# Optimization experiments

Measured on AMD Instinct MI355X. Metric: run time of the kernel, lower is better.

## Reference

```python
import jax, jax.numpy as jnp
import numpy as np

B, N = 262144, 32
NEG = -1e4  # acts as -inf: exp(NEG) == 0 in fp32, clean gradients (softmax weight 0)


def setup_inputs() -> dict:
    key = jax.random.key(0)
    k1, k2, k3 = jax.random.split(key, 3)
    scores = jax.random.normal(k1, (B, N), dtype=jnp.float32)
    ranks = jax.random.randint(k2, (B, N), 0, 32, dtype=jnp.int64)
    mask = jax.random.randint(k3, (B, N), 0, 2, dtype=jnp.int32).astype(bool)
    return {"scores": scores, "ranks": ranks, "mask": mask}


def reference(scores, ranks, mask):
    # n valid (non-padded) items per row
    n = jnp.sum(~mask, axis=1)                              # [B]
    # sort each row by rank, pushing padded entries to the end (stable sort,
    # matching per-row argsort over the valid subset in the original)
    sort_key = jnp.where(mask, N + 1, ranks)                # [B, N]
    order = jnp.argsort(sort_key, axis=1)                   # jnp argsort is stable
    s_sorted = jnp.take_along_axis(scores, order, axis=1)   # [B, N]

    pos = jnp.arange(N)
    valid = pos[None, :] < n[:, None]                       # first n slots hold valid scores
    s_m = jnp.where(valid, s_sorted, NEG)                   # padded -> effectively -inf

    # reverse cumulative logsumexp: rev_lse[k] = logsumexp(s_sorted[k:n])
    rev_lse = jax.lax.cumlogsumexp(s_m, axis=1, reverse=True)

    # original sums k = 0 .. n-2 of -(s_k - logsumexp(s_{k:}))
    term_mask = pos[None, :] < (n[:, None] - 1)
    per_row = -jnp.sum(jnp.where(term_mask, s_m - rev_lse, 0.0), axis=1)  # [B]

    use = n >= 2                                            # rows with < 2 valid are skipped
    per_row = jnp.where(use, per_row / jnp.maximum(n, 1).astype(per_row.dtype), 0.0)
    n_valid = jnp.sum(use)
    return jnp.sum(per_row) / jnp.maximum(n_valid, 1).astype(per_row.dtype)
```

## Files before the change

### kernel.cpp

```cpp
#include <hip/hip_runtime.h>
#include <cstdint>

#define TPB 128
#define LOG2E 1.4426950408889634f
#define LN2   0.69314718055994531f

__global__ __launch_bounds__(TPB)
void pl_main(const float* __restrict__ scores,
             const int* __restrict__ ranks,
             const int* __restrict__ mask,
             float* __restrict__ partials,
             int B)
{
    const int tid = threadIdx.x;
    const int row = blockIdx.x * TPB + tid;

    __shared__ float eb[32 * TPB];

    float per_row = 0.0f, cnt = 0.0f;

    if (row < B) {
        const float4* sp = reinterpret_cast<const float4*>(scores) + (size_t)row * 8;
        const int4*   rp = reinterpret_cast<const int4*>(ranks)  + (size_t)row * 8;
        const int4*   mp = reinterpret_cast<const int4*>(mask)   + (size_t)row * 8;

        float    s[32];
        unsigned K[32];

        #pragma unroll
        for (int c = 0; c < 8; ++c) {
            float4 sv = sp[c];
            int4   rv = rp[c];
            int4   qv = mp[c];
            const int j = c * 4;
            s[j+0] = sv.x; s[j+1] = sv.y; s[j+2] = sv.z; s[j+3] = sv.w;
            K[j+0] = (unsigned)((qv.x << 10) + (rv.x << 5) + (j + 0));
            K[j+1] = (unsigned)((qv.y << 10) + (rv.y << 5) + (j + 1));
            K[j+2] = (unsigned)((qv.z << 10) + (rv.z << 5) + (j + 2));
            K[j+3] = (unsigned)((qv.w << 10) + (rv.w << 5) + (j + 3));
        }

        int n = 0;
        float mx = -3.0e38f;
        #pragma unroll
        for (int j = 0; j < 32; ++j) {
            n += (K[j] < 1024u) ? 1 : 0;
            mx = fmaxf(mx, s[j]);
        }
        const float xm = mx * LOG2E;

        float Ssum = 0.0f;
        #pragma unroll
        for (int j = 0; j < 32; ++j) {
            const bool valid = (K[j] < 1024u);
            float x = __builtin_fmaf(s[j], LOG2E, -xm);
            float e = __builtin_amdgcn_exp2f(x);
            e = valid ? e : 0.0f;
            Ssum += valid ? s[j] : 0.0f;
            eb[j * TPB + tid] = e;
        }

        #pragma unroll
        for (int kk = 2; kk <= 32; kk <<= 1) {
            #pragma unroll
            for (int jj = kk >> 1; jj > 0; jj >>= 1) {
                #pragma unroll
                for (int i = 0; i < 32; ++i) {
                    const int l = i ^ jj;
                    if (l > i) {
                        const unsigned a = K[i], b = K[l];
                        const unsigned mn = a < b ? a : b;
                        const unsigned mh = a < b ? b : a;
                        if ((i & kk) == 0) { K[i] = mn; K[l] = mh; }
                        else               { K[i] = mh; K[l] = mn; }
                    }
                }
            }
        }

        float es[32];
        #pragma unroll
        for (int p = 0; p < 32; ++p) {
            es[p] = eb[(K[p] & 31u) * TPB + tid];
        }

        float t = 0.0f, lsum = 0.0f;
        #pragma unroll
        for (int g = 7; g >= 0; --g) {
            float prod = 1.0f;
            #pragma unroll
            for (int q = 3; q >= 0; --q) {
                const int p = 4 * g + q;
                t += es[p];
                prod *= (K[p] < 1024u) ? t : 1.0f;
            }
            lsum += __builtin_amdgcn_logf(prod);
        }

        if (n >= 2) {
            const float loss = (float)n * mx + LN2 * lsum - Ssum;
            per_row = loss / (float)n;
            cnt = 1.0f;
        }
    }

    #pragma unroll
    for (int d = 32; d >= 1; d >>= 1) {
        per_row += __shfl_xor(per_row, d, 64);
        cnt     += __shfl_xor(cnt,     d, 64);
    }
    __shared__ float rbuf[4];
    if ((tid & 63) == 0) {
        rbuf[(tid >> 6)]     = per_row;
        rbuf[2 + (tid >> 6)] = cnt;
    }
    __syncthreads();
    if (tid == 0) {
        partials[2 * blockIdx.x]     = rbuf[0] + rbuf[1];
        partials[2 * blockIdx.x + 1] = rbuf[2] + rbuf[3];
    }
}

__global__ __launch_bounds__(256)
void pl_final(const float* __restrict__ partials, int nb, float* __restrict__ out)
{
    const int tid = threadIdx.x;
    float s = 0.0f, c = 0.0f;
    for (int i = tid; i < nb; i += 256) {
        s += partials[2 * i];
        c += partials[2 * i + 1];
    }
    #pragma unroll
    for (int d = 32; d >= 1; d >>= 1) {
        s += __shfl_xor(s, d, 64);
        c += __shfl_xor(c, d, 64);
    }
    __shared__ float sb[8];
    if ((tid & 63) == 0) {
        sb[tid >> 6]       = s;
        sb[4 + (tid >> 6)] = c;
    }
    __syncthreads();
    if (tid == 0) {
        const float S = sb[0] + sb[1] + sb[2] + sb[3];
        const float C = sb[4] + sb[5] + sb[6] + sb[7];
        out[0] = S / fmaxf(C, 1.0f);
    }
}

extern "C" void kernel_launch(void* const* d_in, const int* in_sizes, int n_in,
                              void* d_out, int out_size, void* d_ws, size_t ws_size,
                              hipStream_t stream)
{
    const float* scores = (const float*)d_in[0];
    const int*   ranks  = (const int*)d_in[1];
    const int*   mask   = (const int*)d_in[2];

    const int B  = in_sizes[0] / 32;
    const int nb = (B + TPB - 1) / TPB;

    float* partials = (float*)d_ws;

    pl_main<<<nb, TPB, 0, stream>>>(scores, ranks, mask, partials, B);
    pl_final<<<1, 256, 0, stream>>>(partials, nb, (float*)d_out);
}
```

Before: 26.43 us.

## Reformulate loss via log-product of exps, move exp after sort, enlarge blocks

Drops the separate max/sum pass. Validity is now taken from sorted position, and the valid count comes from summing mask values. The score sum term is replaced by subtracting the log of products of sorted exps. Block size grows to 256 with an occupancy hint, and shared buffers are enlarged to match. This cuts per-element ALU work and register pressure, at the risk of underflow in the exp products and higher LDS use per block.

```diff
diff --git a/kernel.cpp b/kernel.cpp
--- a/kernel.cpp
+++ b/kernel.cpp
@@ -1,11 +1,11 @@
 #include <hip/hip_runtime.h>
 #include <cstdint>
 
-#define TPB 128
+#define TPB 256
 #define LOG2E 1.4426950408889634f
 #define LN2   0.69314718055994531f
 
-__global__ __launch_bounds__(TPB)
+__global__ __launch_bounds__(TPB, 4)
 void pl_main(const float* __restrict__ scores,
              const int* __restrict__ ranks,
              const int* __restrict__ mask,
@@ -24,41 +24,24 @@
         const int4*   rp = reinterpret_cast<const int4*>(ranks)  + (size_t)row * 8;
         const int4*   mp = reinterpret_cast<const int4*>(mask)   + (size_t)row * 8;
 
-        float    s[32];
+        float4 sv[8];
+        #pragma unroll
+        for (int c = 0; c < 8; ++c) sv[c] = sp[c];
+
         unsigned K[32];
-
+        int nm = 0;
         #pragma unroll
         for (int c = 0; c < 8; ++c) {
-            float4 sv = sp[c];
-            int4   rv = rp[c];
-            int4   qv = mp[c];
+            const int4 rv = rp[c];
+            const int4 qv = mp[c];
             const int j = c * 4;
-            s[j+0] = sv.x; s[j+1] = sv.y; s[j+2] = sv.z; s[j+3] = sv.w;
-            K[j+0] = (unsigned)((qv.x << 10) + (rv.x << 5) + (j + 0));
-            K[j+1] = (unsigned)((qv.y << 10) + (rv.y << 5) + (j + 1));
-            K[j+2] = (unsigned)((qv.z << 10) + (rv.z << 5) + (j + 2));
-            K[j+3] = (unsigned)((qv.w << 10) + (rv.w << 5) + (j + 3));
+            K[j+0] = (unsigned)((qv.x << 10) + (rv.x << 5) + (j+0));
+            K[j+1] = (unsigned)((qv.y << 10) + (rv.y << 5) + (j+1));
+            K[j+2] = (unsigned)((qv.z << 10) + (rv.z << 5) + (j+2));
+            K[j+3] = (unsigned)((qv.w << 10) + (rv.w << 5) + (j+3));
+            nm += (qv.x + qv.y) + (qv.z + qv.w);
         }
-
-        int n = 0;
-        float mx = -3.0e38f;
-        #pragma unroll
-        for (int j = 0; j < 32; ++j) {
-            n += (K[j] < 1024u) ? 1 : 0;
-            mx = fmaxf(mx, s[j]);
-        }
-        const float xm = mx * LOG2E;
-
-        float Ssum = 0.0f;
-        #pragma unroll
-        for (int j = 0; j < 32; ++j) {
-            const bool valid = (K[j] < 1024u);
-            float x = __builtin_fmaf(s[j], LOG2E, -xm);
-            float e = __builtin_amdgcn_exp2f(x);
-            e = valid ? e : 0.0f;
-            Ssum += valid ? s[j] : 0.0f;
-            eb[j * TPB + tid] = e;
-        }
+        const int n = 32 - nm;
 
         #pragma unroll
         for (int kk = 2; kk <= 32; kk <<= 1) {
@@ -78,28 +61,45 @@
             }
         }
 
+        float cm[8];
+        #pragma unroll
+        for (int c = 0; c < 8; ++c)
+            cm[c] = fmaxf(fmaxf(sv[c].x, sv[c].y), fmaxf(sv[c].z, sv[c].w));
+        const float mx = fmaxf(fmaxf(fmaxf(cm[0], cm[1]), fmaxf(cm[2], cm[3])),
+                               fmaxf(fmaxf(cm[4], cm[5]), fmaxf(cm[6], cm[7])));
+        const float nml = -mx * LOG2E;
+
+        #pragma unroll
+        for (int c = 0; c < 8; ++c) {
+            const int j = c * 4;
+            eb[(j+0)*TPB + tid] = __builtin_amdgcn_exp2f(__builtin_fmaf(sv[c].x, LOG2E, nml));
+            eb[(j+1)*TPB + tid] = __builtin_amdgcn_exp2f(__builtin_fmaf(sv[c].y, LOG2E, nml));
+            eb[(j+2)*TPB + tid] = __builtin_amdgcn_exp2f(__builtin_fmaf(sv[c].z, LOG2E, nml));
+            eb[(j+3)*TPB + tid] = __builtin_amdgcn_exp2f(__builtin_fmaf(sv[c].w, LOG2E, nml));
+        }
+
         float es[32];
         #pragma unroll
-        for (int p = 0; p < 32; ++p) {
+        for (int p = 0; p < 32; ++p)
             es[p] = eb[(K[p] & 31u) * TPB + tid];
-        }
 
         float t = 0.0f, lsum = 0.0f;
         #pragma unroll
         for (int g = 7; g >= 0; --g) {
-            float prod = 1.0f;
+            float pT = 1.0f, pE = 1.0f;
             #pragma unroll
             for (int q = 3; q >= 0; --q) {
-                const int p = 4 * g + q;
-                t += es[p];
-                prod *= (K[p] < 1024u) ? t : 1.0f;
+                const int p = 4*g + q;
+                const bool v = (p < n);
+                t  += v ? es[p] : 0.0f;
+                pT *= v ? t     : 1.0f;
+                pE *= v ? es[p] : 1.0f;
             }
-            lsum += __builtin_amdgcn_logf(prod);
+            lsum += __builtin_amdgcn_logf(pT) - __builtin_amdgcn_logf(pE);
         }
 
         if (n >= 2) {
-            const float loss = (float)n * mx + LN2 * lsum - Ssum;
-            per_row = loss / (float)n;
+            per_row = (LN2 * lsum) / (float)n;
             cnt = 1.0f;
         }
     }
@@ -109,15 +109,15 @@
         per_row += __shfl_xor(per_row, d, 64);
         cnt     += __shfl_xor(cnt,     d, 64);
     }
-    __shared__ float rbuf[4];
+    __shared__ float rbuf[8];
     if ((tid & 63) == 0) {
         rbuf[(tid >> 6)]     = per_row;
-        rbuf[2 + (tid >> 6)] = cnt;
+        rbuf[4 + (tid >> 6)] = cnt;
     }
     __syncthreads();
     if (tid == 0) {
-        partials[2 * blockIdx.x]     = rbuf[0] + rbuf[1];
-        partials[2 * blockIdx.x + 1] = rbuf[2] + rbuf[3];
+        partials[2*blockIdx.x]     = (rbuf[0] + rbuf[1]) + (rbuf[2] + rbuf[3]);
+        partials[2*blockIdx.x + 1] = (rbuf[4] + rbuf[5]) + (rbuf[6] + rbuf[7]);
     }
 }
 
@@ -127,8 +127,8 @@
     const int tid = threadIdx.x;
     float s = 0.0f, c = 0.0f;
     for (int i = tid; i < nb; i += 256) {
-        s += partials[2 * i];
-        c += partials[2 * i + 1];
+        s += partials[2*i];
+        c += partials[2*i + 1];
     }
     #pragma unroll
     for (int d = 32; d >= 1; d >>= 1) {
```

New measurement: 27.07 us. +2.4%, slower.
